# Kernel optimization log

Hardware: AMD Instinct MI355X
Metric: run time of the kernel (lower is better)

The kernel has to match this reference:

```python
import jax, jax.numpy as jnp
import numpy as np

DK, DL, HID = 128, 128, 128  # per init_kwargs: mlp_list=[256,128,128]


def setup_inputs() -> dict:
    key = jax.random.key(0)
    k1, k2, k3, k4, k5 = jax.random.split(key, 5)
    B, K, L = 2, 128, 4096
    inputA = jax.random.normal(k1, (B, K, DK), dtype=jnp.float32)
    inputB = jax.random.normal(k2, (B, L, DL), dtype=jnp.float32)
    # MLP layer 0: Linear(256 -> 128), kaiming-uniform-ish init
    lim1 = 1.0 / np.sqrt(DK + DL)
    W1 = jax.random.uniform(k3, (DK + DL, HID), jnp.float32, -lim1, lim1)
    b1 = jax.random.uniform(k4, (HID,), jnp.float32, -lim1, lim1)
    # scoring Linear(128 -> 1, bias=False)
    lim2 = 1.0 / np.sqrt(HID)
    w2 = jax.random.uniform(k5, (HID,), jnp.float32, -lim2, lim2)
    return {"inputA": inputA, "inputB": inputB, "W1": W1, "b1": b1,
            "w2": w2, "nA": K, "nB": L}


def reference(inputA, inputB, W1, b1, w2, nA, nB):
    # Original: tC = cat([repeat(A), repeat(B)], -1); mlp(tC); linear; softmax(L).
    # Fused-equivalent math: split W1 rows between the A-part and B-part of the
    # concat, so the first Linear is two small matmuls + broadcast add.
    hA = jnp.einsum('bkd,dh->bkh', inputA, W1[:DK])        # (B, K, H)
    hB = jnp.einsum('bld,dh->blh', inputB, W1[DK:])        # (B, L, H)
    h = jax.nn.relu(hA[:, :, None, :] + hB[:, None, :, :] + b1)  # (B, K, L, H)
    scores = jnp.einsum('bklh,h->bkl', h, w2)              # (B, K, L)
    return jax.nn.softmax(scores, axis=2)
```

## Files before the change

### kernel.cpp

```cpp
#include <hip/hip_runtime.h>
#include <hip/hip_fp16.h>
#include <math.h>

constexpr int BB = 2;
constexpr int KK = 128;
constexpr int LL = 4096;
constexpr int DD = 128;
constexpr int HH = 128;

typedef _Float16 f16x2 __attribute__((ext_vector_type(2)));

__device__ __forceinline__ float4 ld4(const float* p) {
    return *reinterpret_cast<const float4*>(p);
}

__device__ __forceinline__ uint32_t pkh2(float a, float b) {
    return __builtin_bit_cast(uint32_t, __floats2half2_rn(a, b));
}

__device__ __forceinline__ uint32_t duph(float x) {
    __half h = __float2half(x);
    unsigned short us = __builtin_bit_cast(unsigned short, h);
    return (uint32_t)us * 0x10001u;
}


__global__ __launch_bounds__(256) void k1_gemm(
    const float* __restrict__ inA, const float* __restrict__ inB,
    const float* __restrict__ W1, const float* __restrict__ b1,
    const float* __restrict__ w2,
    uint32_t* __restrict__ u_dup, uint32_t* __restrict__ w2_dup,
    uint32_t* __restrict__ vT2)
{
    __shared__ __align__(16) char smem[48 * 1024];
    float*  sIn = reinterpret_cast<float*>(smem);
    float4* sW4 = reinterpret_cast<float4*>(smem + 16 * 1024);

    const int bid = blockIdx.x;
    const int tid = threadIdx.x;

    int row0, rows;
    bool isA;
    if (bid < 256) {
        const int x = bid & 7, y = bid >> 3;
        const int C = x + 8 * (y & 1);
        row0 = C * 512 + (y >> 1) * 32;
        rows = 32; isA = false;
    } else {
        row0 = (bid - 256) * 8;
        rows = 8;  isA = true;
    }
    const float* src = (isA ? inA : inB) + (size_t)row0 * DD;
    const float4* wsrc = reinterpret_cast<const float4*>(W1 + (isA ? 0 : DD * HH));

    for (int n = tid; n < rows * 32; n += 256)
        reinterpret_cast<float4*>(sIn)[n] =
            reinterpret_cast<const float4*>(src)[n];

    const int tx = tid & 31;
    const int ty = tid >> 5;
    const bool active = (ty * 4 + 3) < rows;

    float acc[4][4];
    #pragma unroll
    for (int r = 0; r < 4; ++r)
        #pragma unroll
        for (int c = 0; c < 4; ++c) acc[r][c] = 0.f;

    for (int wh = 0; wh < 2; ++wh) {
        __syncthreads();
        #pragma unroll
        for (int q = 0; q < 8; ++q)
            sW4[tid + 256 * q] = wsrc[wh * 2048 + tid + 256 * q];
        __syncthreads();

        if (active) {
            #pragma unroll 2
            for (int dd0 = 0; dd0 < 64; dd0 += 4) {
                const int d0 = wh * 64 + dd0;
                float4 w4[4];
                #pragma unroll
                for (int dd = 0; dd < 4; ++dd)
                    w4[dd] = sW4[(dd0 + dd) * 32 + tx];
                float a[4][4];
                #pragma unroll
                for (int r = 0; r < 4; ++r) {
                    float4 a4 = ld4(&sIn[(ty * 4 + r) * 128 + d0]);
                    a[r][0] = a4.x; a[r][1] = a4.y; a[r][2] = a4.z; a[r][3] = a4.w;
                }
                #pragma unroll
                for (int dd = 0; dd < 4; ++dd) {
                    const float4 wv = w4[dd];
                    #pragma unroll
                    for (int r = 0; r < 4; ++r) {
                        const float av = a[r][dd];
                        acc[r][0] = fmaf(av, wv.x, acc[r][0]);
                        acc[r][1] = fmaf(av, wv.y, acc[r][1]);
                        acc[r][2] = fmaf(av, wv.z, acc[r][2]);
                        acc[r][3] = fmaf(av, wv.w, acc[r][3]);
                    }
                }
            }
        }
    }

    if (isA) {
        if (active) {
            const float4 bb = ld4(&b1[tx * 4]);
            #pragma unroll
            for (int r = 0; r < 4; ++r) {
                uint4 o;
                o.x = duph(acc[r][0] + bb.x);
                o.y = duph(acc[r][1] + bb.y);
                o.z = duph(acc[r][2] + bb.z);
                o.w = duph(acc[r][3] + bb.w);
                *reinterpret_cast<uint4*>(
                    &u_dup[(size_t)(row0 + ty * 4 + r) * HH + tx * 4]) = o;
            }
        }
        if (bid == 256 && tid < HH) w2_dup[tid] = duph(w2[tid]);
    } else {
        const int bsel = row0 >> 12;
        const int lp0  = ((row0 & 4095) + ty * 4) >> 1;
        uint32_t* vb = vT2 + (size_t)bsel * (8 * 2048 * 16);
        #pragma unroll
        for (int c = 0; c < 4; ++c) {
            const int h = tx * 4 + c, g = h >> 4, ph = h & 15;
            uint32_t* dst = vb + ((size_t)g * 2048 + lp0) * 16 + ph;
            dst[0]  = pkh2(acc[0][c], acc[1][c]);
            dst[16] = pkh2(acc[2][c], acc[3][c]);
        }
    }
}

__global__ __launch_bounds__(512) void k2_score(
    const uint32_t* __restrict__ u_dup, const uint32_t* __restrict__ w2_dup,
    const uint32_t* __restrict__ vT2, float* __restrict__ out)
{
    __shared__ __align__(16) uint32_t sU[8 * HH];
    __shared__ __align__(16) uint32_t sW[HH];

    int m = blockIdx.x;
    const int cb = m & 7;   m >>= 3;
    const int kt = m & 15;  m >>= 4;
    const int b  = m;
    const int tid = threadIdx.x;

    if (tid < 256)
        reinterpret_cast<uint4*>(sU)[tid] =
            reinterpret_cast<const uint4*>(u_dup + (size_t)(b * KK + kt * 8) * HH)[tid];
    else if (tid < 288)
        reinterpret_cast<uint4*>(sW)[tid - 256] =
            reinterpret_cast<const uint4*>(w2_dup)[tid - 256];
    __syncthreads();

    const int kh = tid >> 8;
    const int t  = tid & 255;
    const int lp = cb * 256 + t;

    const uint4* vg = reinterpret_cast<const uint4*>(
                          vT2 + ((size_t)b * 8 * 2048 + lp) * 16);
    const uint4* su4 = reinterpret_cast<const uint4*>(sU + kh * 4 * HH);
    const uint4* sw4 = reinterpret_cast<const uint4*>(sW);

    const f16x2 hz = { (_Float16)0, (_Float16)0 };
    float2 facc[4];
    #pragma unroll
    for (int k = 0; k < 4; ++k) { facc[k].x = 0.f; facc[k].y = 0.f; }

    #pragma unroll
    for (int g = 0; g < 8; ++g) {
        uint4 vq[4];
        #pragma unroll
        for (int c = 0; c < 4; ++c)
            vq[c] = vg[(size_t)g * 8192 + c];
        const uint32_t* vd = reinterpret_cast<const uint32_t*>(vq);

        uint4 wq[4];
        #pragma unroll
        for (int c = 0; c < 4; ++c) wq[c] = sw4[g * 4 + c];
        const uint32_t* wd = reinterpret_cast<const uint32_t*>(wq);

        f16x2 hacc[4] = { hz, hz, hz, hz };
        #pragma unroll
        for (int k = 0; k < 4; ++k) {
            uint4 uq[4];
            #pragma unroll
            for (int c = 0; c < 4; ++c) uq[c] = su4[k * 32 + g * 4 + c];
            const uint32_t* ud = reinterpret_cast<const uint32_t*>(uq);
            #pragma unroll
            for (int ph = 0; ph < 16; ++ph) {
                f16x2 vv = __builtin_bit_cast(f16x2, vd[ph]);
                f16x2 uu = __builtin_bit_cast(f16x2, ud[ph]);
                f16x2 ww = __builtin_bit_cast(f16x2, wd[ph]);
                f16x2 s = vv + uu;
                s = __builtin_elementwise_max(s, hz);
                hacc[k] = s * ww + hacc[k];
            }
        }
        #pragma unroll
        for (int k = 0; k < 4; ++k) {
            facc[k].x += (float)hacc[k].x;
            facc[k].y += (float)hacc[k].y;
        }
    }

    #pragma unroll
    for (int k = 0; k < 4; ++k)
        *reinterpret_cast<float2*>(
            &out[(size_t)(b * KK + kt * 8 + kh * 4 + k) * LL + 2 * lp]) = facc[k];
}

__global__ __launch_bounds__(1024) void k3_softmax(float* __restrict__ out)
{
    __shared__ float reds[16];

    const int row = blockIdx.x;
    float* p = out + (size_t)row * LL;
    const int tid = threadIdx.x;

    float4 x = reinterpret_cast<const float4*>(p)[tid];

    x.x = expf(x.x); x.y = expf(x.y);
    x.z = expf(x.z); x.w = expf(x.w);
    float s = (x.x + x.y) + (x.z + x.w);
    #pragma unroll
    for (int off = 32; off > 0; off >>= 1)
        s += __shfl_xor(s, off, 64);
    const int lane = tid & 63, wv = tid >> 6;
    if (lane == 0) reds[wv] = s;
    __syncthreads();
    if (tid < 16) {
        float ss = reds[tid];
        #pragma unroll
        for (int off = 8; off > 0; off >>= 1)
            ss += __shfl_xor(ss, off, 64);
        reds[tid] = ss;
    }
    __syncthreads();
    s = reds[0];

    const float inv = 1.0f / s;
    x.x *= inv; x.y *= inv; x.z *= inv; x.w *= inv;
    reinterpret_cast<float4*>(p)[tid] = x;
}

extern "C" void kernel_launch(void* const* d_in, const int* in_sizes, int n_in,
                              void* d_out, int out_size, void* d_ws, size_t ws_size,
                              hipStream_t stream)
{
    const float* inA = (const float*)d_in[0];
    const float* inB = (const float*)d_in[1];
    const float* W1  = (const float*)d_in[2];
    const float* b1  = (const float*)d_in[3];
    const float* w2  = (const float*)d_in[4];
    float* out = (float*)d_out;

    char* ws = (char*)d_ws;
    uint32_t* u_dup  = (uint32_t*)ws;
    uint32_t* w2_dup = (uint32_t*)(ws + 0x20000);
    uint32_t* vT2    = (uint32_t*)(ws + 0x40000);

    hipLaunchKernelGGL(k1_gemm, dim3(288), dim3(256), 0, stream,
                       inA, inB, W1, b1, w2, u_dup, w2_dup, vT2);
    hipLaunchKernelGGL(k2_score, dim3(256), dim3(512), 0, stream,
                       u_dup, w2_dup, vT2, out);
    hipLaunchKernelGGL(k3_softmax, dim3(BB * KK), dim3(1024), 0, stream, out);
}
```

Baseline: 27.93 us.

## Fuse softmax into score kernel with cross-block partial-sum barrier

```diff
diff --git a/kernel.cpp b/kernel.cpp
--- a/kernel.cpp
+++ b/kernel.cpp
@@ -30,7 +30,7 @@
     const float* __restrict__ W1, const float* __restrict__ b1,
     const float* __restrict__ w2,
     uint32_t* __restrict__ u_dup, uint32_t* __restrict__ w2_dup,
-    uint32_t* __restrict__ vT2)
+    uint32_t* __restrict__ vT2, int* __restrict__ sync_ctrs)
 {
     __shared__ __align__(16) char smem[48 * 1024];
     float*  sIn = reinterpret_cast<float*>(smem);
@@ -38,6 +38,8 @@
 
     const int bid = blockIdx.x;
     const int tid = threadIdx.x;
+
+    if (bid == 287 && tid < 64) sync_ctrs[tid] = 0;
 
     int row0, rows;
     bool isA;
@@ -133,18 +135,23 @@
     }
 }
 
-__global__ __launch_bounds__(512) void k2_score(
+__global__ __launch_bounds__(512) void k2_fused(
     const uint32_t* __restrict__ u_dup, const uint32_t* __restrict__ w2_dup,
-    const uint32_t* __restrict__ vT2, float* __restrict__ out)
+    const uint32_t* __restrict__ vT2, float* __restrict__ psum,
+    int* __restrict__ arrive, int* __restrict__ done,
+    float* __restrict__ out)
 {
     __shared__ __align__(16) uint32_t sU[8 * HH];
     __shared__ __align__(16) uint32_t sW[HH];
+    __shared__ float red[8][4];
+    __shared__ float sS[8];
 
     int m = blockIdx.x;
     const int cb = m & 7;   m >>= 3;
     const int kt = m & 15;  m >>= 4;
     const int b  = m;
     const int tid = threadIdx.x;
+    const int grp = b * 16 + kt;
 
     if (tid < 256)
         reinterpret_cast<uint4*>(sU)[tid] =
@@ -205,44 +212,75 @@
         }
     }
 
-    #pragma unroll
-    for (int k = 0; k < 4; ++k)
+    float2 te[4];
+    #pragma unroll
+    for (int k = 0; k < 4; ++k) {
+        te[k].x = expf(facc[k].x);
+        te[k].y = expf(facc[k].y);
+    }
+
+    const int wave = tid >> 6, lane = tid & 63;
+    float ps[4];
+    #pragma unroll
+    for (int k = 0; k < 4; ++k) {
+        ps[k] = te[k].x + te[k].y;
+        #pragma unroll
+        for (int off = 32; off > 0; off >>= 1)
+            ps[k] += __shfl_xor(ps[k], off, 64);
+    }
+    if (lane == 0) {
+        red[wave][0] = ps[0]; red[wave][1] = ps[1];
+        red[wave][2] = ps[2]; red[wave][3] = ps[3];
+    }
+    __syncthreads();
+    if (tid < 8) {
+        const int khh = tid >> 2, kk = tid & 3;
+        const float S = (red[khh * 4 + 0][kk] + red[khh * 4 + 1][kk])
+                      + (red[khh * 4 + 2][kk] + red[khh * 4 + 3][kk]);
+        psum[(size_t)(grp * 8 + khh * 4 + kk) * 8 + cb] = S;
+    }
+    __syncthreads();
+
+    if (tid == 0) {
+        __threadfence();
+        __hip_atomic_fetch_add(&arrive[grp], 1, __ATOMIC_ACQ_REL,
+                               __HIP_MEMORY_SCOPE_AGENT);
+        while (__hip_atomic_load(&arrive[grp], __ATOMIC_ACQUIRE,
+                                 __HIP_MEMORY_SCOPE_AGENT) < 8)
+            __builtin_amdgcn_s_sleep(1);
+    }
+    __syncthreads();
+
+    if (tid < 8) {
+        float S = 0.f;
+        #pragma unroll
+        for (int c = 0; c < 8; ++c)
+            S += __hip_atomic_load(&psum[(size_t)(grp * 8 + tid) * 8 + c],
+                                   __ATOMIC_RELAXED, __HIP_MEMORY_SCOPE_AGENT);
+        sS[tid] = S;
+    }
+    __syncthreads();
+
+    #pragma unroll
+    for (int k = 0; k < 4; ++k) {
+        const float inv = 1.0f / sS[kh * 4 + k];
+        float2 o;
+        o.x = te[k].x * inv;
+        o.y = te[k].y * inv;
         *reinterpret_cast<float2*>(
-            &out[(size_t)(b * KK + kt * 8 + kh * 4 + k) * LL + 2 * lp]) = facc[k];
-}
-
-__global__ __launch_bounds__(1024) void k3_softmax(float* __restrict__ out)
-{
-    __shared__ float reds[16];
-
-    const int row = blockIdx.x;
-    float* p = out + (size_t)row * LL;
-    const int tid = threadIdx.x;
-
-    float4 x = reinterpret_cast<const float4*>(p)[tid];
-
-    x.x = expf(x.x); x.y = expf(x.y);
-    x.z = expf(x.z); x.w = expf(x.w);
-    float s = (x.x + x.y) + (x.z + x.w);
-    #pragma unroll
-    for (int off = 32; off > 0; off >>= 1)
-        s += __shfl_xor(s, off, 64);
-    const int lane = tid & 63, wv = tid >> 6;
-    if (lane == 0) reds[wv] = s;
-    __syncthreads();
-    if (tid < 16) {
-        float ss = reds[tid];
-        #pragma unroll
-        for (int off = 8; off > 0; off >>= 1)
-            ss += __shfl_xor(ss, off, 64);
-        reds[tid] = ss;
-    }
-    __syncthreads();
-    s = reds[0];
-
-    const float inv = 1.0f / s;
-    x.x *= inv; x.y *= inv; x.z *= inv; x.w *= inv;
-    reinterpret_cast<float4*>(p)[tid] = x;
+            &out[(size_t)(b * KK + kt * 8 + kh * 4 + k) * LL + 2 * lp]) = o;
+    }
+
+    if (tid == 0) {
+        const int d = __hip_atomic_fetch_add(&done[grp], 1, __ATOMIC_ACQ_REL,
+                                             __HIP_MEMORY_SCOPE_AGENT);
+        if (d == 7) {
+            __hip_atomic_store(&arrive[grp], 0, __ATOMIC_RELAXED,
+                               __HIP_MEMORY_SCOPE_AGENT);
+            __hip_atomic_store(&done[grp], 0, __ATOMIC_RELAXED,
+                               __HIP_MEMORY_SCOPE_AGENT);
+        }
+    }
 }
 
 extern "C" void kernel_launch(void* const* d_in, const int* in_sizes, int n_in,
@@ -260,10 +298,13 @@
     uint32_t* u_dup  = (uint32_t*)ws;
     uint32_t* w2_dup = (uint32_t*)(ws + 0x20000);
     uint32_t* vT2    = (uint32_t*)(ws + 0x40000);
+    float*    psum   = (float*)(ws + 0x240000);
+    int*      ctrs   = (int*)(ws + 0x242000);
+    int*      arrive = ctrs;
+    int*      done   = ctrs + 32;
 
     hipLaunchKernelGGL(k1_gemm, dim3(288), dim3(256), 0, stream,
-                       inA, inB, W1, b1, w2, u_dup, w2_dup, vT2);
-    hipLaunchKernelGGL(k2_score, dim3(256), dim3(512), 0, stream,
-                       u_dup, w2_dup, vT2, out);
-    hipLaunchKernelGGL(k3_softmax, dim3(BB * KK), dim3(1024), 0, stream, out);
-}
+                       inA, inB, W1, b1, w2, u_dup, w2_dup, vT2, ctrs);
+    hipLaunchKernelGGL(k2_fused, dim3(256), dim3(512), 0, stream,
+                       u_dup, w2_dup, vT2, psum, arrive, done, out);
+}
```

New measurement: 45.03 us. +61.2%, slower.
